# Kernel tuning notes

Hardware: AMD Instinct MI355X
Metric: run time of the kernel (lower is better)

The kernel has to match this reference:

```python
import jax, jax.numpy as jnp
import numpy as np

B, N, M, K = 4, 16384, 16384, 16   # batch, points, centers, neighbors
C, O, G = 64, 64, 8                # in_planes, out_planes, group


def setup_inputs() -> dict:
    key = jax.random.key(0)
    ks = jax.random.split(key, 16)
    r = lambda i, sh, s=1.0: jax.random.normal(ks[i], sh, jnp.float32) * s
    return dict(
        center_pos=r(0, (B, M, 3)),
        center_fea=r(1, (B, C, M)),
        pos=r(2, (B, N, 3)),
        fea=r(3, (B, C, N)),
        idx=jax.random.randint(ks[4], (B, M, K), 0, N, jnp.int32),
        # linear q/k/v
        Wq=r(5, (C, O), 0.05), bq=jnp.zeros((O,), jnp.float32),
        Wk=r(6, (C, O), 0.05), bk=jnp.zeros((O,), jnp.float32),
        Wv=r(7, (C, O), 0.05), bv=jnp.zeros((O,), jnp.float32),
        # center_pos_encode: conv1x1(3->O, no bias) + folded BN (scale,shift) + relu + conv1x1(O->O)
        cpe_w1=r(8, (3, O), 0.05), cpe_s=jnp.ones((O,), jnp.float32), cpe_b=jnp.zeros((O,), jnp.float32),
        cpe_w2=r(9, (O, O), 0.05), cpe_b2=jnp.zeros((O,), jnp.float32),
        # pos_encode (Conv2d 1x1 == per-point linear)
        pe_w1=r(10, (3, O), 0.05), pe_s=jnp.ones((O,), jnp.float32), pe_b=jnp.zeros((O,), jnp.float32),
        pe_w2=r(11, (O, O), 0.05), pe_b2=jnp.zeros((O,), jnp.float32),
        # weight_encode (O -> G)
        we_w1=r(12, (O, G), 0.05), we_s=jnp.ones((G,), jnp.float32), we_b=jnp.zeros((G,), jnp.float32),
        we_w2=r(13, (G, G), 0.05), we_b2=jnp.zeros((G,), jnp.float32),
    )


def _mlp2(x, w1, s, b, w2, b2):
    # conv1x1(no bias) -> inference BatchNorm folded to (scale, shift) -> ReLU -> conv1x1(+bias)
    h = jax.nn.relu(x @ w1 * s + b)
    return h @ w2 + b2


def reference(center_pos, center_fea, pos, fea, idx,
              Wq, bq, Wk, bk, Wv, bv,
              cpe_w1, cpe_s, cpe_b, cpe_w2, cpe_b2,
              pe_w1, pe_s, pe_b, pe_w2, pe_b2,
              we_w1, we_s, we_b, we_w2, we_b2):
    x_q = center_fea.transpose(0, 2, 1) @ Wq + bq        # [B,M,O]
    ft = fea.transpose(0, 2, 1)                          # [B,N,C]
    x_k = ft @ Wk + bk                                   # [B,N,O]
    x_v = ft @ Wv + bv                                   # [B,N,O]

    gather = jax.vmap(lambda a, i: a[i])                 # per-batch irregular gather
    nk = gather(x_k, idx)                                # [B,M,K,O]
    nv = gather(x_v, idx)                                # [B,M,K,O]
    npos = gather(pos, idx) - center_pos[:, :, None, :]  # [B,M,K,3] relative coords

    cpr = _mlp2(center_pos, cpe_w1, cpe_s, cpe_b, cpe_w2, cpe_b2)  # [B,M,O]
    pr = _mlp2(npos, pe_w1, pe_s, pe_b, pe_w2, pe_b2)              # [B,M,K,O]

    r_qk = nk - x_q[:, :, None, :] + cpr[:, :, None, :]  # [B,M,K,O]
    v = nv + pr                                          # [B,M,K,O]

    w = _mlp2(r_qk, we_w1, we_s, we_b, we_w2, we_b2)     # [B,M,K,G]
    w = jax.nn.softmax(w, axis=2)                        # softmax over neighbors

    v = v.reshape(B, M, K, G, O // G)
    out = jnp.einsum('bmkgi,bmkg->bmgi', v, w).reshape(B, M, O)
    return out.transpose(0, 2, 1)                        # [B,O,M]
```

## Files before the change

### kernel.cpp

```cpp
#include <hip/hip_runtime.h>
#include <hip/hip_bf16.h>

typedef unsigned short u16;
typedef __attribute__((ext_vector_type(8))) __bf16 bf8v;
typedef __attribute__((ext_vector_type(8))) _Float16 f16x8;
typedef __attribute__((ext_vector_type(2))) _Float16 h2v;
typedef __attribute__((ext_vector_type(4))) float f32x4;
typedef __attribute__((ext_vector_type(4))) unsigned uint4v;

#define B_ 4
#define N_ 16384
#define M_ 16384
#define K_ 16
#define C_ 64
#define O_ 64
#define G_ 8

__device__ __forceinline__ float bf2f(u16 x){
  union { unsigned u; float f; } v; v.u = ((unsigned)x) << 16; return v.f;
}
__device__ __forceinline__ u16 f2bf(float f){
  union { float f; unsigned u; } v; v.f = f;
  unsigned u = v.u;
  return (u16)((u + 0x7FFFu + ((u >> 16) & 1u)) >> 16);
}
__device__ __forceinline__ u16 f2h(float f){
  union { _Float16 h; u16 u; } v; v.h = (_Float16)f; return v.u;
}
__device__ __forceinline__ h2v mkh2(float a, float b){
  h2v r = {(_Float16)a, (_Float16)b}; return r;
}

__global__ __launch_bounds__(256) void pre_kernel(
    const float* __restrict__ center_pos, const float* __restrict__ center_fea,
    const float* __restrict__ pos, const float* __restrict__ fea,
    const float* __restrict__ Wq, const float* __restrict__ bq,
    const float* __restrict__ Wk, const float* __restrict__ bk,
    const float* __restrict__ Wv, const float* __restrict__ bv,
    const float* __restrict__ cpe_w1, const float* __restrict__ cpe_s, const float* __restrict__ cpe_b,
    const float* __restrict__ cpe_w2, const float* __restrict__ cpe_b2,
    const float* __restrict__ we_w1,
    u16* __restrict__ xk, u16* __restrict__ xv, float* __restrict__ qw,
    float* __restrict__ pos4, float* __restrict__ cp4)
{
  __shared__ u16 sWT[128*72];
  __shared__ u16 sA[64*72];
  __shared__ u16 sOut[64*136];
  __shared__ float sMisc[256];
  __shared__ float sCi[8];
  int tid = threadIdx.x;
  int l = tid & 63, w = tid >> 6, c = l & 15, q = l >> 4;
  int blk = blockIdx.x;

  if (blk < 256){
    int P0 = blk * 256; int b = P0 >> 14; int n00 = P0 & (N_-1);
    const float* fb = fea + (long)b*C_*N_;
    for (int e = tid; e < 8192; e += 256){
      int k = e >> 7, col = e & 127;
      float v = (col < 64) ? Wk[k*64 + col] : Wv[k*64 + (col-64)];
      sWT[col*72 + k] = f2bf(v);
    }
    if (tid < 128) sMisc[tid] = (tid < 64) ? bk[tid] : bv[tid-64];
    {
      long pg = (long)P0 + tid;
      f32x4 r = {pos[pg*3], pos[pg*3+1], pos[pg*3+2], 0.f};
      ((f32x4*)pos4)[pg] = r;
    }

    #pragma unroll 1
    for (int s = 0; s < 4; s++){
      int n0 = n00 + s*64;
      #pragma unroll
      for (int pp = 0; pp < 4; pp++){
        int k = pp*16 + (tid >> 4);
        int nf = (tid & 15)*4;
        f32x4 v = *(const f32x4*)&fb[(long)k*N_ + n0 + nf];
        sA[(nf+0)*72+k] = f2bf(v[0]); sA[(nf+1)*72+k] = f2bf(v[1]);
        sA[(nf+2)*72+k] = f2bf(v[2]); sA[(nf+3)*72+k] = f2bf(v[3]);
      }
      __syncthreads();

      bf8v af0 = *(const bf8v*)&sA[(w*16+c)*72 + q*8];
      bf8v af1 = *(const bf8v*)&sA[(w*16+c)*72 + 32 + q*8];
      f32x4 acc[8];
      #pragma unroll
      for (int t = 0; t < 8; t++){
        float bb = sMisc[16*t + c];
        f32x4 a_ = {bb, bb, bb, bb};
        bf8v b0 = *(const bf8v*)&sWT[(16*t + c)*72 + q*8];
        bf8v b1 = *(const bf8v*)&sWT[(16*t + c)*72 + 32 + q*8];
        a_ = __builtin_amdgcn_mfma_f32_16x16x32_bf16(af0, b0, a_, 0,0,0);
        a_ = __builtin_amdgcn_mfma_f32_16x16x32_bf16(af1, b1, a_, 0,0,0);
        acc[t] = a_;
      }
      #pragma unroll
      for (int t = 0; t < 8; t++)
        #pragma unroll
        for (int r = 0; r < 4; r++)
          sOut[(w*16 + q*4 + r)*136 + 16*t + c] = f2bf(acc[t][r]);
      __syncthreads();

      #pragma unroll
      for (int rep = 0; rep < 4; rep++){
        int chunk = rep*256 + tid;
        int pt = chunk >> 4, c8i = chunk & 15;
        uint4v val = *(const uint4v*)&sOut[pt*136 + c8i*8];
        int col8 = c8i*8;
        long row = (long)P0 + s*64 + pt;
        if (col8 < 64) *(uint4v*)(xk + row*64 + col8)      = val;
        else           *(uint4v*)(xv + row*64 + (col8-64)) = val;
      }
      __syncthreads();
    }
  } else {
    int P0 = (blk - 256) * 256; int b = P0 >> 14; int m00 = P0 & (M_-1);
    const float* cfb = center_fea + (long)b*C_*M_;
    float* sWe = (float*)sOut;
    float* sQ  = (float*)sOut;
    for (int e = tid; e < 512; e += 256) sWe[e] = we_w1[e];
    if (tid < 64){
      float sc = cpe_s[tid];
      sMisc[tid]     = cpe_w1[tid]*sc;
      sMisc[64+tid]  = cpe_w1[64+tid]*sc;
      sMisc[128+tid] = cpe_w1[128+tid]*sc;
      sMisc[192+tid] = cpe_b[tid];
    }
    {
      long pg = (long)P0 + tid;
      f32x4 r = {center_pos[pg*3], center_pos[pg*3+1], center_pos[pg*3+2], 0.f};
      ((f32x4*)cp4)[pg] = r;
    }
    __syncthreads();
    {
      int k = tid >> 1, g0 = (tid & 1)*4;
      const float* brow = (k < 64) ? (cpe_w2 + k*64) : (Wq + (k-64)*64);
      float sgn = (k < 64) ? 1.f : -1.f;
      float aw[4] = {0.f,0.f,0.f,0.f};
      for (int o = 0; o < 64; o++){
        float bo = brow[o]*sgn;
        #pragma unroll
        for (int gg=0; gg<4; gg++) aw[gg] += bo * sWe[o*8 + g0+gg];
      }
      #pragma unroll
      for (int gg=0; gg<4; gg++) sWT[(g0+gg)*136 + k] = f2bf(aw[gg]);
    }
    for (int e = tid; e < 2176; e += 256){
      int r = e / 136, cc = e % 136;
      if (r >= 8 || cc >= 128) sWT[e] = 0;
    }
    if (tid < 8){
      float s = 0.f;
      for (int o = 0; o < 64; o++) s += (cpe_b2[o] - bq[o]) * sWe[o*8 + tid];
      sCi[tid] = s;
    }
    __syncthreads();

    #pragma unroll 1
    for (int s = 0; s < 4; s++){
      int m0 = m00 + s*64;
      #pragma unroll
      for (int pp = 0; pp < 4; pp++){
        int k = pp*16 + (tid >> 4);
        int nf = (tid & 15)*4;
        f32x4 v = *(const f32x4*)&cfb[(long)k*M_ + m0 + nf];
        sA[(nf+0)*72+k] = f2bf(v[0]); sA[(nf+1)*72+k] = f2bf(v[1]);
        sA[(nf+2)*72+k] = f2bf(v[2]); sA[(nf+3)*72+k] = f2bf(v[3]);
      }
      long c3 = (long)(P0 + s*64 + w*16 + c)*3;
      float cp0 = center_pos[c3], cp1 = center_pos[c3+1], cp2 = center_pos[c3+2];
      __syncthreads();

      bf8v ah[2];
      #pragma unroll
      for (int ks = 0; ks < 2; ks++){
        union { bf8v v; u16 sv[8]; } ua;
        #pragma unroll
        for (int j = 0; j < 8; j++){
          int h = ks*32 + q*8 + j;
          float hv = cp0*sMisc[h] + cp1*sMisc[64+h] + cp2*sMisc[128+h] + sMisc[192+h];
          ua.sv[j] = f2bf(fmaxf(hv, 0.f));
        }
        ah[ks] = ua.v;
      }
      bf8v acf0 = *(const bf8v*)&sA[(w*16+c)*72 + q*8];
      bf8v acf1 = *(const bf8v*)&sA[(w*16+c)*72 + 32 + q*8];

      float ci = (c < 8) ? sCi[c] : 0.f;
      f32x4 aq = {ci, ci, ci, ci};
      {
        bf8v b0 = *(const bf8v*)&sWT[c*136 + q*8];
        bf8v b1 = *(const bf8v*)&sWT[c*136 + 32 + q*8];
        bf8v b2 = *(const bf8v*)&sWT[c*136 + 64 + q*8];
        bf8v b3 = *(const bf8v*)&sWT[c*136 + 96 + q*8];
        aq = __builtin_amdgcn_mfma_f32_16x16x32_bf16(ah[0], b0, aq, 0,0,0);
        aq = __builtin_amdgcn_mfma_f32_16x16x32_bf16(ah[1], b1, aq, 0,0,0);
        aq = __builtin_amdgcn_mfma_f32_16x16x32_bf16(acf0,  b2, aq, 0,0,0);
        aq = __builtin_amdgcn_mfma_f32_16x16x32_bf16(acf1,  b3, aq, 0,0,0);
      }
      __syncthreads();
      if (c < 8){
        #pragma unroll
        for (int r = 0; r < 4; r++) sQ[(w*16 + q*4 + r)*8 + c] = aq[r];
      }
      __syncthreads();
      for (int e = tid; e < 512; e += 256)
        qw[(long)(P0 + s*64)*8 + e] = sQ[e];
      __syncthreads();
    }
  }
}

__global__ __launch_bounds__(256) void attn_kernel(
    const float* __restrict__ cp4, const float* __restrict__ pos4,
    const int* __restrict__ idx,
    const float* __restrict__ pe_w1, const float* __restrict__ pe_s, const float* __restrict__ pe_b,
    const float* __restrict__ pe_w2, const float* __restrict__ pe_b2,
    const float* __restrict__ we_w1, const float* __restrict__ we_s, const float* __restrict__ we_b,
    const float* __restrict__ we_w2, const float* __restrict__ we_b2,
    const u16* __restrict__ xk, const u16* __restrict__ xv, const float* __restrict__ qw,
    float* __restrict__ out)
{
  int tid = threadIdx.x;
  __shared__ float s_w1f[192], s_pb[64], s_pb2[64], s_ww2[64];
  __shared__ float s_ws8[8], s_wb8[8], s_wb28[8];
  __shared__ f32x4 s_dyn4[768];
  __shared__ float s_tile[32*66];

  char* dynb = (char*)s_dyn4;

  if (tid < 64){
    float sc = pe_s[tid];
    s_w1f[tid]     = pe_w1[tid]*sc;
    s_w1f[64+tid]  = pe_w1[64+tid]*sc;
    s_w1f[128+tid] = pe_w1[128+tid]*sc;
    s_pb[tid]  = pe_b[tid];
    s_pb2[tid] = pe_b2[tid];
    s_ww2[tid] = we_w2[tid];
  }
  if (tid >= 64 && tid < 72){
    int g = tid-64;
    s_ws8[g]=we_s[g]; s_wb8[g]=we_b[g]; s_wb28[g]=we_b2[g];
  }
  u16* stg = (u16*)dynb;
  #pragma unroll
  for (int pp = 0; pp < 4; pp++){
    int row = pp*16 + (tid >> 4);
    int colf = (tid & 15)*4;
    f32x4 v = *(const f32x4*)&pe_w2[row*64 + colf];
    stg[(colf+0)*72+row] = f2h(v[0]); stg[(colf+1)*72+row] = f2h(v[1]);
    stg[(colf+2)*72+row] = f2h(v[2]); stg[(colf+3)*72+row] = f2h(v[3]);
  }
  u16* stg2 = (u16*)(dynb + 9216);
  for (int e = tid; e < 512; e += 256){
    int k = e >> 3, cc = e & 7;
    stg2[cc*72 + k] = f2bf(we_w1[e]);
  }
  for (int e = tid; e < 576; e += 256) stg2[576 + e] = 0;
  __syncthreads();

  int w = tid >> 6, l = tid & 63, c = l & 15, q = l >> 4, c8 = c & 7;

  f16x8 pw2f[4][2];
  bf8v ww1f[2];
  f16x8 w2B, hz8;
  #pragma unroll
  for (int t = 0; t < 4; t++){
    pw2f[t][0] = *(const f16x8*)&stg[(t*16+c)*72 + q*8];
    pw2f[t][1] = *(const f16x8*)&stg[(t*16+c)*72 + 32 + q*8];
  }
  ww1f[0] = *(const bf8v*)&stg2[c*72 + q*8];
  ww1f[1] = *(const bf8v*)&stg2[c*72 + 32 + q*8];
  {
    union { f16x8 v; u16 s[8]; } uu;
    #pragma unroll
    for (int j = 0; j < 8; j++)
      uu.s[j] = (q == 0 && c < 8) ? f2h(s_ww2[j*8 + c]) : (u16)0;
    w2B = uu.v;
    #pragma unroll
    for (int j = 0; j < 8; j++) uu.s[j] = 0;
    hz8 = uu.v;
  }
  h2v cw0[2][4], cw1[2][4], cw2[2][4], cb[2][4];
  #pragma unroll
  for (int ks = 0; ks < 2; ks++)
    #pragma unroll
    for (int jj = 0; jj < 4; jj++){
      int o = ks*32 + q*8 + jj*2;
      cw0[ks][jj] = mkh2(s_w1f[o],     s_w1f[o+1]);
      cw1[ks][jj] = mkh2(s_w1f[64+o],  s_w1f[65+o]);
      cw2[ks][jj] = mkh2(s_w1f[128+o], s_w1f[129+o]);
      cb [ks][jj] = mkh2(s_pb[o],      s_pb[o+1]);
    }
  float ws_c = s_ws8[c8], wb_c = s_wb8[c8], wb2_c = s_wb28[c8];
  float pb2l = s_pb2[l];
  h2v hz2 = {(_Float16)0.f, (_Float16)0.f};
  __syncthreads();

  u16*  sv16 = (u16*) (dynb + w*3072);
  float* swt = (float*)(dynb + w*3072 + 2176);
  u16*  sh   = (u16*) (dynb + w*3072 + 2816);

  int blk = blockIdx.x;
  int pbase = (((blk & 7) << 8) | (blk >> 3)) * 32;
  int b = pbase >> 14;
  const u16* xkb = xk + (long)b * N_ * 64;
  const u16* xvb = xv + (long)b * N_ * 64;
  const f32x4* pos4b = ((const f32x4*)pos4) + (long)b * N_;
  int ch = c >> 3;
  int gl = l >> 3;

  int pb0 = pbase + w*8;
  const int*   idxl = idx + (long)pb0*16 + c;
  const float* qwl  = qw  + (long)pb0*8 + c8;
  const f32x4* cp4l = ((const f32x4*)cp4) + pb0;

  int iv0 = idxl[0];
  int ivt = idxl[16];
  int iv2 = idxl[32];
  float q0 = qwl[0], q1 = qwl[8], q2 = qwl[16];
  f32x4 cpv = cp4l[0];
  f32x4 ppA = pos4b[iv0];
  const u16* krA = xkb + (size_t)iv0*64;
  bf8v kaA0 = *(const bf8v*)(krA + q*8);
  bf8v kaA1 = *(const bf8v*)(krA + 32 + q*8);
  const u16* vrA = xvb + (size_t)iv0*64;
  uint4v vaA0 = *(const uint4v*)(vrA + q*8);
  uint4v vaA1 = *(const uint4v*)(vrA + 32 + q*8);
  f32x4 ppB = pos4b[ivt];
  const u16* krB = xkb + (size_t)ivt*64;
  bf8v kaB0 = *(const bf8v*)(krB + q*8);
  bf8v kaB1 = *(const bf8v*)(krB + 32 + q*8);
  const u16* vrB = xvb + (size_t)ivt*64;
  uint4v vaB0 = *(const uint4v*)(vrB + q*8);
  uint4v vaB1 = *(const uint4v*)(vrB + 32 + q*8);

  #pragma unroll 1
  for (int i = 0; i < 8; i++){
    f32x4 ppN = pos4b[iv2];
    const u16* krN = xkb + (size_t)iv2*64;
    bf8v kaN0 = *(const bf8v*)(krN + q*8);
    bf8v kaN1 = *(const bf8v*)(krN + 32 + q*8);
    const u16* vrN = xvb + (size_t)iv2*64;
    uint4v vaN0 = *(const uint4v*)(vrN + q*8);
    uint4v vaN1 = *(const uint4v*)(vrN + 32 + q*8);
    int ni = (i < 7) ? i+1 : 7;
    f32x4 cpn = cp4l[ni];
    int n3 = (i < 5) ? i+3 : 7;
    int iv3 = idxl[n3*16];
    float q3 = qwl[n3*8];

    *(uint4v*)&sv16[c*68 + q*8]      = vaA0;
    *(uint4v*)&sv16[c*68 + 32 + q*8] = vaA1;

    float np0 = ppA[0] - cpv[0], np1 = ppA[1] - cpv[1], np2 = ppA[2] - cpv[2];
    h2v np0h = {(_Float16)np0, (_Float16)np0};
    h2v np1h = {(_Float16)np1, (_Float16)np1};
    h2v np2h = {(_Float16)np2, (_Float16)np2};
    f16x8 h1f[2];
    #pragma unroll
    for (int ks = 0; ks < 2; ks++){
      union { f16x8 v; h2v p[4]; } hu;
      #pragma unroll
      for (int jj = 0; jj < 4; jj++){
        h2v a = cb[ks][jj];
        a = np0h*cw0[ks][jj] + a;
        a = np1h*cw1[ks][jj] + a;
        a = np2h*cw2[ks][jj] + a;
        hu.p[jj] = __builtin_elementwise_max(a, hz2);
      }
      h1f[ks] = hu.v;
    }

    f32x4 h2a = {q0, q0, q0, q0};
    h2a = __builtin_amdgcn_mfma_f32_16x16x32_bf16(kaA0, ww1f[0], h2a, 0,0,0);
    h2a = __builtin_amdgcn_mfma_f32_16x16x32_bf16(kaA1, ww1f[1], h2a, 0,0,0);

    if (c < 8){
      #pragma unroll
      for (int r = 0; r < 4; r++)
        sh[(q*4+r)*8 + c] = f2h(fmaxf(h2a[r]*ws_c + wb_c, 0.f));
    }
    f16x8 hrow = *(const f16x8*)&sh[c*8];
    f16x8 ahf = (q == 0) ? hrow : hz8;

    f32x4 wlv = {wb2_c, wb2_c, wb2_c, wb2_c};
    wlv = __builtin_amdgcn_mfma_f32_16x16x32_f16(ahf, w2B, wlv, 0,0,0);

    float e0 = exp2f(wlv[0]*1.44269504f);
    float e1 = exp2f(wlv[1]*1.44269504f);
    float e2 = exp2f(wlv[2]*1.44269504f);
    float e3 = exp2f(wlv[3]*1.44269504f);
    float sm = e0+e1+e2+e3;
    sm += __shfl_xor(sm, 16, 64);
    sm += __shfl_xor(sm, 32, 64);
    float rn = 1.0f / sm;
    if (c < 8){
      f32x4 ev = {e0*rn, e1*rn, e2*rn, e3*rn};
      *(f32x4*)&swt[c*20 + q*4] = ev;
    }

    float ov[4];
    #pragma unroll
    for (int t = 0; t < 4; t++){
      f32x4 z = {0.f,0.f,0.f,0.f};
      z = __builtin_amdgcn_mfma_f32_16x16x32_f16(h1f[0], pw2f[t][0], z, 0,0,0);
      z = __builtin_amdgcn_mfma_f32_16x16x32_f16(h1f[1], pw2f[t][1], z, 0,0,0);
      f32x4 wv = *(const f32x4*)&swt[(t*2+ch)*20 + q*4];
      ov[t] = z[0]*wv[0] + z[1]*wv[1] + z[2]*wv[2] + z[3]*wv[3];
    }
    #pragma unroll
    for (int t = 0; t < 4; t++){
      ov[t] += __shfl_xor(ov[t], 16, 64);
      ov[t] += __shfl_xor(ov[t], 32, 64);
    }
    float ovsel = ov[0];
    ovsel = (q==1) ? ov[1] : ovsel;
    ovsel = (q==2) ? ov[2] : ovsel;
    ovsel = (q==3) ? ov[3] : ovsel;

    float vacc = 0.f;
    {
      const f32x4* wr4 = (const f32x4*)&swt[gl*20];
      const u16* svl = &sv16[l];
      #pragma unroll
      for (int k4 = 0; k4 < 4; k4++){
        f32x4 wv = wr4[k4];
        vacc += bf2f(svl[(4*k4+0)*68])*wv[0];
        vacc += bf2f(svl[(4*k4+1)*68])*wv[1];
        vacc += bf2f(svl[(4*k4+2)*68])*wv[2];
        vacc += bf2f(svl[(4*k4+3)*68])*wv[3];
      }
    }

    s_tile[(w*8+i)*66 + l] = ovsel + vacc + pb2l;

    kaA0 = kaB0; kaA1 = kaB1; vaA0 = vaB0; vaA1 = vaB1; ppA = ppB;
    kaB0 = kaN0; kaB1 = kaN1; vaB0 = vaN0; vaB1 = vaN1; ppB = ppN;
    cpv = cpn;
    iv2 = iv3; q0 = q1; q1 = q2; q2 = q3;
  }
  __syncthreads();

  int o0 = tid >> 5, pt = tid & 31;
  int m0 = pbase & (M_-1);
  long outb = ((long)b*64) * M_ + m0 + pt;
  #pragma unroll
  for (int ii = 0; ii < 8; ii++){
    int o = o0*8 + ii;
    out[outb + (long)o*M_] = s_tile[pt*66 + o];
  }
}

extern "C" void kernel_launch(void* const* d_in, const int* in_sizes, int n_in,
                              void* d_out, int out_size, void* d_ws, size_t ws_size,
                              hipStream_t stream) {
  const float* center_pos = (const float*)d_in[0];
  const float* center_fea = (const float*)d_in[1];
  const float* pos        = (const float*)d_in[2];
  const float* fea        = (const float*)d_in[3];
  const int*   idx        = (const int*)d_in[4];
  const float* Wq = (const float*)d_in[5];   const float* bq = (const float*)d_in[6];
  const float* Wk = (const float*)d_in[7];   const float* bk = (const float*)d_in[8];
  const float* Wv = (const float*)d_in[9];   const float* bv = (const float*)d_in[10];
  const float* cpe_w1 = (const float*)d_in[11]; const float* cpe_s = (const float*)d_in[12];
  const float* cpe_b  = (const float*)d_in[13]; const float* cpe_w2 = (const float*)d_in[14];
  const float* cpe_b2 = (const float*)d_in[15];
  const float* pe_w1 = (const float*)d_in[16]; const float* pe_s = (const float*)d_in[17];
  const float* pe_b  = (const float*)d_in[18]; const float* pe_w2 = (const float*)d_in[19];
  const float* pe_b2 = (const float*)d_in[20];
  const float* we_w1 = (const float*)d_in[21]; const float* we_s = (const float*)d_in[22];
  const float* we_b  = (const float*)d_in[23]; const float* we_w2 = (const float*)d_in[24];
  const float* we_b2 = (const float*)d_in[25];

  const size_t SZ = (size_t)B_*N_*64;
  u16* xk = (u16*)d_ws;
  u16* xv = xk + SZ;
  float* qwp = (float*)(xv + SZ);
  float* pos4p = qwp + (size_t)B_*M_*8;
  float* cp4p  = pos4p + (size_t)B_*N_*4;
  float* outp = (float*)d_out;

  hipLaunchKernelGGL(pre_kernel, dim3(512), dim3(256), 0, stream,
      center_pos, center_fea, pos, fea, Wq, bq, Wk, bk, Wv, bv,
      cpe_w1, cpe_s, cpe_b, cpe_w2, cpe_b2, we_w1,
      xk, xv, qwp, pos4p, cp4p);
  hipLaunchKernelGGL(attn_kernel, dim3(2048), dim3(256), 0, stream,
      cp4p, pos4p, idx, pe_w1, pe_s, pe_b, pe_w2, pe_b2,
      we_w1, we_s, we_b, we_w2, we_b2, xk, xv, qwp, outp);
}
```

Baseline: 206.7 us.

## Process two center points per loop iteration with doubled shared staging buffers

The per-wave loop now handles two center points (a and b) per iteration instead of one, interleaving their MFMA, softmax, shuffle and LDS work. The gather prefetch becomes two points ahead for each stream, and the per-wave LDS staging area is doubled so each point has its own buffers. The aim is more independent work per iteration to hide gather latency and MFMA/LDS dependency stalls. In exchange it raises register pressure and LDS use, which may lower occupancy.

New measurement: 210.0 us. No clear change (+1.6%).

```diff
diff --git a/kernel.cpp b/kernel.cpp
--- a/kernel.cpp
+++ b/kernel.cpp
@@ -223,7 +223,7 @@
   int tid = threadIdx.x;
   __shared__ float s_w1f[192], s_pb[64], s_pb2[64], s_ww2[64];
   __shared__ float s_ws8[8], s_wb8[8], s_wb28[8];
-  __shared__ f32x4 s_dyn4[768];
+  __shared__ f32x4 s_dyn4[1536];
   __shared__ float s_tile[32*66];
 
   char* dynb = (char*)s_dyn4;
@@ -296,9 +296,12 @@
   h2v hz2 = {(_Float16)0.f, (_Float16)0.f};
   __syncthreads();
 
-  u16*  sv16 = (u16*) (dynb + w*3072);
-  float* swt = (float*)(dynb + w*3072 + 2176);
-  u16*  sh   = (u16*) (dynb + w*3072 + 2816);
+  u16*  sva  = (u16*) (dynb + w*6144);
+  float* swta = (float*)(dynb + w*6144 + 2176);
+  u16*  sha  = (u16*) (dynb + w*6144 + 2816);
+  u16*  svb  = (u16*) (dynb + w*6144 + 3072);
+  float* swtb = (float*)(dynb + w*6144 + 5248);
+  u16*  shb  = (u16*) (dynb + w*6144 + 5888);
 
   int blk = blockIdx.x;
   int pbase = (((blk & 7) << 8) | (blk >> 3)) * 32;
@@ -314,130 +317,186 @@
   const float* qwl  = qw  + (long)pb0*8 + c8;
   const f32x4* cp4l = ((const f32x4*)cp4) + pb0;
 
-  int iv0 = idxl[0];
-  int ivt = idxl[16];
-  int iv2 = idxl[32];
-  float q0 = qwl[0], q1 = qwl[8], q2 = qwl[16];
-  f32x4 cpv = cp4l[0];
-  f32x4 ppA = pos4b[iv0];
-  const u16* krA = xkb + (size_t)iv0*64;
-  bf8v kaA0 = *(const bf8v*)(krA + q*8);
-  bf8v kaA1 = *(const bf8v*)(krA + 32 + q*8);
-  const u16* vrA = xvb + (size_t)iv0*64;
-  uint4v vaA0 = *(const uint4v*)(vrA + q*8);
-  uint4v vaA1 = *(const uint4v*)(vrA + 32 + q*8);
-  f32x4 ppB = pos4b[ivt];
-  const u16* krB = xkb + (size_t)ivt*64;
-  bf8v kaB0 = *(const bf8v*)(krB + q*8);
-  bf8v kaB1 = *(const bf8v*)(krB + 32 + q*8);
-  const u16* vrB = xvb + (size_t)ivt*64;
-  uint4v vaB0 = *(const uint4v*)(vrB + q*8);
-  uint4v vaB1 = *(const uint4v*)(vrB + 32 + q*8);
+  int iva = idxl[0];
+  int ivb = idxl[16];
+  int iv2a = idxl[32];
+  int iv2b = idxl[48];
+  float qa = qwl[0], qb = qwl[8];
+  f32x4 cpa = cp4l[0], cpb = cp4l[1];
+
+  f32x4 ppa = pos4b[iva];
+  const u16* kra = xkb + (size_t)iva*64;
+  bf8v kaa0 = *(const bf8v*)(kra + q*8);
+  bf8v kaa1 = *(const bf8v*)(kra + 32 + q*8);
+  const u16* vra = xvb + (size_t)iva*64;
+  uint4v vaa0 = *(const uint4v*)(vra + q*8);
+  uint4v vaa1 = *(const uint4v*)(vra + 32 + q*8);
+
+  f32x4 ppb = pos4b[ivb];
+  const u16* krb = xkb + (size_t)ivb*64;
+  bf8v kab0 = *(const bf8v*)(krb + q*8);
+  bf8v kab1 = *(const bf8v*)(krb + 32 + q*8);
+  const u16* vrb = xvb + (size_t)ivb*64;
+  uint4v vab0 = *(const uint4v*)(vrb + q*8);
+  uint4v vab1 = *(const uint4v*)(vrb + 32 + q*8);
 
   #pragma unroll 1
-  for (int i = 0; i < 8; i++){
-    f32x4 ppN = pos4b[iv2];
-    const u16* krN = xkb + (size_t)iv2*64;
-    bf8v kaN0 = *(const bf8v*)(krN + q*8);
-    bf8v kaN1 = *(const bf8v*)(krN + 32 + q*8);
-    const u16* vrN = xvb + (size_t)iv2*64;
-    uint4v vaN0 = *(const uint4v*)(vrN + q*8);
-    uint4v vaN1 = *(const uint4v*)(vrN + 32 + q*8);
-    int ni = (i < 7) ? i+1 : 7;
-    f32x4 cpn = cp4l[ni];
-    int n3 = (i < 5) ? i+3 : 7;
-    int iv3 = idxl[n3*16];
-    float q3 = qwl[n3*8];
-
-    *(uint4v*)&sv16[c*68 + q*8]      = vaA0;
-    *(uint4v*)&sv16[c*68 + 32 + q*8] = vaA1;
-
-    float np0 = ppA[0] - cpv[0], np1 = ppA[1] - cpv[1], np2 = ppA[2] - cpv[2];
-    h2v np0h = {(_Float16)np0, (_Float16)np0};
-    h2v np1h = {(_Float16)np1, (_Float16)np1};
-    h2v np2h = {(_Float16)np2, (_Float16)np2};
-    f16x8 h1f[2];
+  for (int ii = 0; ii < 4; ii++){
+    int i0 = 2*ii, i1 = 2*ii+1;
+    f32x4 ppna = pos4b[iv2a];
+    const u16* krna = xkb + (size_t)iv2a*64;
+    bf8v kana0 = *(const bf8v*)(krna + q*8);
+    bf8v kana1 = *(const bf8v*)(krna + 32 + q*8);
+    const u16* vrna = xvb + (size_t)iv2a*64;
+    uint4v vana0 = *(const uint4v*)(vrna + q*8);
+    uint4v vana1 = *(const uint4v*)(vrna + 32 + q*8);
+    f32x4 ppnb = pos4b[iv2b];
+    const u16* krnb = xkb + (size_t)iv2b*64;
+    bf8v kanb0 = *(const bf8v*)(krnb + q*8);
+    bf8v kanb1 = *(const bf8v*)(krnb + 32 + q*8);
+    const u16* vrnb = xvb + (size_t)iv2b*64;
+    uint4v vanb0 = *(const uint4v*)(vrnb + q*8);
+    uint4v vanb1 = *(const uint4v*)(vrnb + 32 + q*8);
+    int na = (ii < 3) ? i0+2 : 7, nb = (ii < 3) ? i1+2 : 7;
+    f32x4 cpna = cp4l[na], cpnb = cp4l[nb];
+    float qna = qwl[na*8], qnb = qwl[nb*8];
+    int n4 = (ii < 2) ? i0+4 : 7, n5 = (ii < 2) ? i1+4 : 7;
+    int iv4a = idxl[n4*16], iv4b = idxl[n5*16];
+
+    *(uint4v*)&sva[c*68 + q*8]      = vaa0;
+    *(uint4v*)&sva[c*68 + 32 + q*8] = vaa1;
+    *(uint4v*)&svb[c*68 + q*8]      = vab0;
+    *(uint4v*)&svb[c*68 + 32 + q*8] = vab1;
+
+    float na0 = ppa[0]-cpa[0], na1 = ppa[1]-cpa[1], na2 = ppa[2]-cpa[2];
+    float nb0 = ppb[0]-cpb[0], nb1 = ppb[1]-cpb[1], nb2 = ppb[2]-cpb[2];
+    h2v na0h = {(_Float16)na0,(_Float16)na0}, na1h = {(_Float16)na1,(_Float16)na1}, na2h = {(_Float16)na2,(_Float16)na2};
+    h2v nb0h = {(_Float16)nb0,(_Float16)nb0}, nb1h = {(_Float16)nb1,(_Float16)nb1}, nb2h = {(_Float16)nb2,(_Float16)nb2};
+    f16x8 h1fa[2], h1fb[2];
     #pragma unroll
     for (int ks = 0; ks < 2; ks++){
-      union { f16x8 v; h2v p[4]; } hu;
+      union { f16x8 v; h2v p[4]; } hua, hub;
       #pragma unroll
       for (int jj = 0; jj < 4; jj++){
-        h2v a = cb[ks][jj];
-        a = np0h*cw0[ks][jj] + a;
-        a = np1h*cw1[ks][jj] + a;
-        a = np2h*cw2[ks][jj] + a;
-        hu.p[jj] = __builtin_elementwise_max(a, hz2);
-      }
-      h1f[ks] = hu.v;
-    }
-
-    f32x4 h2a = {q0, q0, q0, q0};
-    h2a = __builtin_amdgcn_mfma_f32_16x16x32_bf16(kaA0, ww1f[0], h2a, 0,0,0);
-    h2a = __builtin_amdgcn_mfma_f32_16x16x32_bf16(kaA1, ww1f[1], h2a, 0,0,0);
+        h2v aa = cb[ks][jj];
+        aa = na0h*cw0[ks][jj] + aa;
+        aa = na1h*cw1[ks][jj] + aa;
+        aa = na2h*cw2[ks][jj] + aa;
+        hua.p[jj] = __builtin_elementwise_max(aa, hz2);
+        h2v ab = cb[ks][jj];
+        ab = nb0h*cw0[ks][jj] + ab;
+        ab = nb1h*cw1[ks][jj] + ab;
+        ab = nb2h*cw2[ks][jj] + ab;
+        hub.p[jj] = __builtin_elementwise_max(ab, hz2);
+      }
+      h1fa[ks] = hua.v;
+      h1fb[ks] = hub.v;
+    }
+
+    f32x4 h2aa = {qa, qa, qa, qa};
+    h2aa = __builtin_amdgcn_mfma_f32_16x16x32_bf16(kaa0, ww1f[0], h2aa, 0,0,0);
+    h2aa = __builtin_amdgcn_mfma_f32_16x16x32_bf16(kaa1, ww1f[1], h2aa, 0,0,0);
+    f32x4 h2ab = {qb, qb, qb, qb};
+    h2ab = __builtin_amdgcn_mfma_f32_16x16x32_bf16(kab0, ww1f[0], h2ab, 0,0,0);
+    h2ab = __builtin_amdgcn_mfma_f32_16x16x32_bf16(kab1, ww1f[1], h2ab, 0,0,0);
 
     if (c < 8){
       #pragma unroll
-      for (int r = 0; r < 4; r++)
-        sh[(q*4+r)*8 + c] = f2h(fmaxf(h2a[r]*ws_c + wb_c, 0.f));
-    }
-    f16x8 hrow = *(const f16x8*)&sh[c*8];
-    f16x8 ahf = (q == 0) ? hrow : hz8;
-
-    f32x4 wlv = {wb2_c, wb2_c, wb2_c, wb2_c};
-    wlv = __builtin_amdgcn_mfma_f32_16x16x32_f16(ahf, w2B, wlv, 0,0,0);
-
-    float e0 = exp2f(wlv[0]*1.44269504f);
-    float e1 = exp2f(wlv[1]*1.44269504f);
-    float e2 = exp2f(wlv[2]*1.44269504f);
-    float e3 = exp2f(wlv[3]*1.44269504f);
-    float sm = e0+e1+e2+e3;
-    sm += __shfl_xor(sm, 16, 64);
-    sm += __shfl_xor(sm, 32, 64);
-    float rn = 1.0f / sm;
+      for (int r = 0; r < 4; r++){
+        sha[(q*4+r)*8 + c] = f2h(fmaxf(h2aa[r]*ws_c + wb_c, 0.f));
+        shb[(q*4+r)*8 + c] = f2h(fmaxf(h2ab[r]*ws_c + wb_c, 0.f));
+      }
+    }
+    f16x8 hrowa = *(const f16x8*)&sha[c*8];
+    f16x8 hrowb = *(const f16x8*)&shb[c*8];
+    f16x8 ahfa = (q == 0) ? hrowa : hz8;
+    f16x8 ahfb = (q == 0) ? hrowb : hz8;
+
+    f32x4 wlva = {wb2_c, wb2_c, wb2_c, wb2_c};
+    wlva = __builtin_amdgcn_mfma_f32_16x16x32_f16(ahfa, w2B, wlva, 0,0,0);
+    f32x4 wlvb = {wb2_c, wb2_c, wb2_c, wb2_c};
+    wlvb = __builtin_amdgcn_mfma_f32_16x16x32_f16(ahfb, w2B, wlvb, 0,0,0);
+
+    float ea0 = exp2f(wlva[0]*1.44269504f);
+    float ea1 = exp2f(wlva[1]*1.44269504f);
+    float ea2 = exp2f(wlva[2]*1.44269504f);
+    float ea3 = exp2f(wlva[3]*1.44269504f);
+    float eb0 = exp2f(wlvb[0]*1.44269504f);
+    float eb1 = exp2f(wlvb[1]*1.44269504f);
+    float eb2 = exp2f(wlvb[2]*1.44269504f);
+    float eb3 = exp2f(wlvb[3]*1.44269504f);
+    float sma = ea0+ea1+ea2+ea3;
+    float smb = eb0+eb1+eb2+eb3;
+    sma += __shfl_xor(sma, 16, 64);
+    smb += __shfl_xor(smb, 16, 64);
+    sma += __shfl_xor(sma, 32, 64);
+    smb += __shfl_xor(smb, 32, 64);
+    float rna = 1.0f / sma;
+    float rnb = 1.0f / smb;
     if (c < 8){
-      f32x4 ev = {e0*rn, e1*rn, e2*rn, e3*rn};
-      *(f32x4*)&swt[c*20 + q*4] = ev;
-    }
-
-    float ov[4];
+      f32x4 eva = {ea0*rna, ea1*rna, ea2*rna, ea3*rna};
+      *(f32x4*)&swta[c*20 + q*4] = eva;
+      f32x4 evb = {eb0*rnb, eb1*rnb, eb2*rnb, eb3*rnb};
+      *(f32x4*)&swtb[c*20 + q*4] = evb;
+    }
+
+    float ova[4], ovb[4];
     #pragma unroll
     for (int t = 0; t < 4; t++){
-      f32x4 z = {0.f,0.f,0.f,0.f};
-      z = __builtin_amdgcn_mfma_f32_16x16x32_f16(h1f[0], pw2f[t][0], z, 0,0,0);
-      z = __builtin_amdgcn_mfma_f32_16x16x32_f16(h1f[1], pw2f[t][1], z, 0,0,0);
-      f32x4 wv = *(const f32x4*)&swt[(t*2+ch)*20 + q*4];
-      ov[t] = z[0]*wv[0] + z[1]*wv[1] + z[2]*wv[2] + z[3]*wv[3];
+      f32x4 za = {0.f,0.f,0.f,0.f};
+      za = __builtin_amdgcn_mfma_f32_16x16x32_f16(h1fa[0], pw2f[t][0], za, 0,0,0);
+      za = __builtin_amdgcn_mfma_f32_16x16x32_f16(h1fa[1], pw2f[t][1], za, 0,0,0);
+      f32x4 wva = *(const f32x4*)&swta[(t*2+ch)*20 + q*4];
+      ova[t] = za[0]*wva[0] + za[1]*wva[1] + za[2]*wva[2] + za[3]*wva[3];
+      f32x4 zb = {0.f,0.f,0.f,0.f};
+      zb = __builtin_amdgcn_mfma_f32_16x16x32_f16(h1fb[0], pw2f[t][0], zb, 0,0,0);
+      zb = __builtin_amdgcn_mfma_f32_16x16x32_f16(h1fb[1], pw2f[t][1], zb, 0,0,0);
+      f32x4 wvb = *(const f32x4*)&swtb[(t*2+ch)*20 + q*4];
+      ovb[t] = zb[0]*wvb[0] + zb[1]*wvb[1] + zb[2]*wvb[2] + zb[3]*wvb[3];
     }
     #pragma unroll
     for (int t = 0; t < 4; t++){
-      ov[t] += __shfl_xor(ov[t], 16, 64);
-      ov[t] += __shfl_xor(ov[t], 32, 64);
-    }
-    float ovsel = ov[0];
-    ovsel = (q==1) ? ov[1] : ovsel;
-    ovsel = (q==2) ? ov[2] : ovsel;
-    ovsel = (q==3) ? ov[3] : ovsel;
-
-    float vacc = 0.f;
+      ova[t] += __shfl_xor(ova[t], 16, 64);
+      ovb[t] += __shfl_xor(ovb[t], 16, 64);
+      ova[t] += __shfl_xor(ova[t], 32, 64);
+      ovb[t] += __shfl_xor(ovb[t], 32, 64);
+    }
+    float ovsela = ova[0];
+    ovsela = (q==1) ? ova[1] : ovsela;
+    ovsela = (q==2) ? ova[2] : ovsela;
+    ovsela = (q==3) ? ova[3] : ovsela;
+    float ovselb = ovb[0];
+    ovselb = (q==1) ? ovb[1] : ovselb;
+    ovselb = (q==2) ? ovb[2] : ovselb;
+    ovselb = (q==3) ? ovb[3] : ovselb;
+
+    float vacca = 0.f, vaccb = 0.f;
     {
-      const f32x4* wr4 = (const f32x4*)&swt[gl*20];
-      const u16* svl = &sv16[l];
+      const f32x4* wr4a = (const f32x4*)&swta[gl*20];
+      const f32x4* wr4b = (const f32x4*)&swtb[gl*20];
+      const u16* svla = &sva[l];
+      const u16* svlb = &svb[l];
       #pragma unroll
       for (int k4 = 0; k4 < 4; k4++){
-        f32x4 wv = wr4[k4];
-        vacc += bf2f(svl[(4*k4+0)*68])*wv[0];
-        vacc += bf2f(svl[(4*k4+1)*68])*wv[1];
-        vacc += bf2f(svl[(4*k4+2)*68])*wv[2];
-        vacc += bf2f(svl[(4*k4+3)*68])*wv[3];
-      }
-    }
-
-    s_tile[(w*8+i)*66 + l] = ovsel + vacc + pb2l;
-
-    kaA0 = kaB0; kaA1 = kaB1; vaA0 = vaB0; vaA1 = vaB1; ppA = ppB;
-    kaB0 = kaN0; kaB1 = kaN1; vaB0 = vaN0; vaB1 = vaN1; ppB = ppN;
-    cpv = cpn;
-    iv2 = iv3; q0 = q1; q1 = q2; q2 = q3;
+        f32x4 wva = wr4a[k4];
+        f32x4 wvb = wr4b[k4];
+        vacca += bf2f(svla[(4*k4+0)*68])*wva[0];
+        vaccb += bf2f(svlb[(4*k4+0)*68])*wvb[0];
+        vacca += bf2f(svla[(4*k4+1)*68])*wva[1];
+        vaccb += bf2f(svlb[(4*k4+1)*68])*wvb[1];
+        vacca += bf2f(svla[(4*k4+2)*68])*wva[2];
+        vaccb += bf2f(svlb[(4*k4+2)*68])*wvb[2];
+        vacca += bf2f(svla[(4*k4+3)*68])*wva[3];
+        vaccb += bf2f(svlb[(4*k4+3)*68])*wvb[3];
+      }
+    }
+
+    s_tile[(w*8+i0)*66 + l] = ovsela + vacca + pb2l;
+    s_tile[(w*8+i1)*66 + l] = ovselb + vaccb + pb2l;
+
+    kaa0 = kana0; kaa1 = kana1; vaa0 = vana0; vaa1 = vana1; ppa = ppna; cpa = cpna; qa = qna;
+    kab0 = kanb0; kab1 = kanb1; vab0 = vanb0; vab1 = vanb1; ppb = ppnb; cpb = cpnb; qb = qnb;
+    iv2a = iv4a; iv2b = iv4b;
   }
   __syncthreads();
 
```
